# Optimization experiments

Hardware: AMD Instinct MI355X
Metric: run time of the kernel (lower is better)

Reference implementation:

```python
import jax, jax.numpy as jnp
import numpy as np

N_HEADS = 64
HEAD_DIM = 128
TOPK = 2048
CHUNK = 256          # indexer_max_chunk_size analogue (Q-block chunking)
FP8_MAX = 448.0      # e4m3 max


def _hadamard_matrix(n):
    H = np.array([[1.0]], dtype=np.float32)
    while H.shape[0] < n:
        H = np.block([[H, H], [H, -H]])
    return jnp.asarray(H, dtype=jnp.float32)

_HM = _hadamard_matrix(HEAD_DIM)


def rotate_activation(x):
    # hadamard_transform(x, scale=hidden^-0.5)
    return (x @ _HM) * (HEAD_DIM ** -0.5)


def _fp8_quant(x):
    # per-last-dim-block (block == head_dim == 128) dynamic fp8 e4m3 quantization
    amax = jnp.max(jnp.abs(x), axis=-1, keepdims=True)
    scale = jnp.maximum(amax, 1e-4) / FP8_MAX
    xq = (x / scale).astype(jnp.float8_e4m3fn).astype(jnp.float32)
    # straight-through: value == quantized, gradient == identity
    xq = x / scale + jax.lax.stop_gradient(xq - x / scale)
    return xq, scale


def setup_inputs() -> dict:
    key = jax.random.key(0)
    k1, k2, k3 = jax.random.split(key, 3)
    T = 4096
    q = jax.random.normal(k1, (T, N_HEADS, HEAD_DIM), dtype=jnp.float32)
    k = jax.random.normal(k2, (T, HEAD_DIM), dtype=jnp.float32)
    weights = jax.random.uniform(k3, (T, N_HEADS), dtype=jnp.float32)
    seq_lens = jnp.full((2,), 2048, dtype=jnp.int32)  # 2 packed sequences
    return {"q": q, "k": k, "weights": weights, "seq_lens": seq_lens}


def reference(q, k, weights, seq_lens):
    T, H, D = q.shape

    # 1) Hadamard rotation of q and k activations
    qr = rotate_activation(q)           # [T, H, D]
    kr = rotate_activation(k)           # [T, D]

    # 2) fp8 quantization with per-(token,head) / per-token scales
    qf, q_scale = _fp8_quant(qr)        # qf [T,H,D], q_scale [T,H,1]
    kf, k_scale = _fp8_quant(kr)        # kf [T,D],   k_scale [T,1]

    # 3) _scale: fold q scales + softmax scale into routing weights
    softmax_scale = D ** -0.5
    w = weights * q_scale[..., 0] * softmax_scale   # [T, H]

    # 4) causal KV bounds per packed token (compute_cu_seqlen_kv_bounds_nocache)
    offs = jnp.concatenate([jnp.zeros(1, jnp.int32), jnp.cumsum(seq_lens).astype(jnp.int32)])
    batch_ids = jnp.repeat(jnp.arange(seq_lens.shape[0], dtype=jnp.int32), seq_lens,
                           total_repeat_length=T)
    cu_ks = offs[batch_ids]                          # start of own sequence
    pos = jnp.arange(T, dtype=jnp.int32)
    cu_ke = pos + 1                                  # causal end (exclusive)

    # 5) chunked indexer logits: I[t,s] = k_scale[s] * sum_h w[t,h]*relu(qf[t,h]Âkf[s])
    n_chunks = T // CHUNK
    q_chunks = qf.reshape(n_chunks, CHUNK, H, D)
    w_chunks = w.reshape(n_chunks, CHUNK, H)

    def body(carry, inp):
        qc, wc = inp                                  # [C,H,D], [C,H]
        sc = jnp.einsum('chd,sd->chs', qc, kf)        # fp8-style GEMM
        lc = jnp.einsum('ch,chs->cs', wc, jax.nn.relu(sc))
        return carry, lc

    _, lg = jax.lax.scan(body, None, (q_chunks, w_chunks))
    logits = lg.reshape(T, T) * k_scale[:, 0][None, :]

    # 6) causal mask from bounds, then top-k KV selection
    mask = (pos[None, :] >= cu_ks[:, None]) & (pos[None, :] < cu_ke[:, None])
    masked = jnp.where(mask, logits, -jnp.inf)
    _, topk_idx = jax.lax.top_k(masked, TOPK)
    return masked, topk_idx.astype(jnp.int32)
```

## Files before the change

### kernel.cpp

```cpp
#include <hip/hip_runtime.h>
#include <stdint.h>

#define HEADS 64
#define HD 128
#define TOPK_N 2048
#define BT 32
#define BS 256
#define XCAP 256

typedef float f32x4 __attribute__((ext_vector_type(4)));
typedef long  lx2  __attribute__((ext_vector_type(2)));

static constexpr float RSQRT_D = 0.08838834764831845f;

__device__ inline unsigned short pk_fp8(float a, float b) {
    int r = __builtin_amdgcn_cvt_pk_fp8_f32(a, b, 0, false);
    return (unsigned short)(r & 0xffff);
}

__device__ inline int perm_src_lane(int m) {
    return ((m & 0x0C) << 2) | ((m & 0x30) >> 2) | (m & 3);
}

__device__ inline void fwht128(float& a, float& b, int lane) {
    float na = a + b, nb = a - b;
    a = na; b = nb;
#pragma unroll
    for (int m = 1; m < 64; m <<= 1) {
        float pa = __shfl_xor(a, m, 64);
        float pb = __shfl_xor(b, m, 64);
        bool hi = (lane & m) != 0;
        a = hi ? (pa - a) : (a + pa);
        b = hi ? (pb - b) : (b + pb);
    }
}

__global__ __launch_bounds__(256)
void k_rotquant(const float* __restrict__ kin, uint8_t* __restrict__ kf,
                float* __restrict__ k_scale, int T) {
    int wave = (int)((blockIdx.x * blockDim.x + threadIdx.x) >> 6);
    int lane = threadIdx.x & 63;
    if (wave >= T) return;
    const float2 v = ((const float2*)(kin + (size_t)wave * HD))[lane];
    float a = v.x, b = v.y;
    fwht128(a, b, lane);
    a *= RSQRT_D; b *= RSQRT_D;
    float amax = fmaxf(fabsf(a), fabsf(b));
#pragma unroll
    for (int m = 1; m < 64; m <<= 1) amax = fmaxf(amax, __shfl_xor(amax, m, 64));
    float scale = fmaxf(amax, 1e-4f) / 448.0f;
    int pk = (int)pk_fp8(a / scale, b / scale);
    int g = __shfl(pk, perm_src_lane(lane), 64);
    *(unsigned short*)(kf + (size_t)wave * HD + lane * 2) = (unsigned short)g;
    if (lane == 0) k_scale[wave] = scale;
}

__global__ __launch_bounds__(256)
void q_rotquant(const float* __restrict__ q, const float* __restrict__ weights,
                uint8_t* __restrict__ qh, float* __restrict__ wprime, int T) {
    int row = (int)((blockIdx.x * blockDim.x + threadIdx.x) >> 6);
    int lane = threadIdx.x & 63;
    if (row >= T * HEADS) return;
    int t = row >> 6, h = row & 63;
    const float2 v = ((const float2*)(q + (size_t)row * HD))[lane];
    float a = v.x, b = v.y;
    fwht128(a, b, lane);
    a *= RSQRT_D; b *= RSQRT_D;
    float amax = fmaxf(fabsf(a), fabsf(b));
#pragma unroll
    for (int m = 1; m < 64; m <<= 1) amax = fmaxf(amax, __shfl_xor(amax, m, 64));
    float scale = fmaxf(amax, 1e-4f) / 448.0f;
    int tb = t >> 5, r = t & 31;
    int pk = (int)pk_fp8(a / scale, b / scale);
    int g = __shfl(pk, perm_src_lane(lane), 64);
    size_t dst = ((((size_t)tb * HEADS + h) << 5) + r) * HD + lane * 2;
    *(unsigned short*)(qh + dst) = (unsigned short)g;
    if (lane == 0) wprime[row] = (weights[row] * scale) * RSQRT_D;
}

__global__ void bounds_kernel(const int* __restrict__ seq_lens, int B,
                              int* __restrict__ cu_ks, int T) {
    __shared__ int offs[130];
    if (threadIdx.x == 0) {
        int acc = 0; offs[0] = 0;
        for (int b = 0; b < B && b < 128; b++) { acc += seq_lens[b]; offs[b + 1] = acc; }
    }
    __syncthreads();
    int t = blockIdx.x * blockDim.x + threadIdx.x;
    if (t < T) {
        int b = 0;
        while (b < B - 1 && offs[b + 1] <= t) b++;
        cu_ks[t] = offs[b];
    }
}

__global__ __launch_bounds__(128)
void queue_kernel(const int* __restrict__ cu_ks, int* __restrict__ tiles,
                  int* __restrict__ cnt, int T) {
    int nb = T / BT;
    int tid = threadIdx.x;
    int x = tid >> 4, i = tid & 15;
    int y = i * 8 + x;
    int c = 0, sbmin = 0;
    if (y < nb) {
        int t0 = y * BT;
        sbmin = cu_ks[t0] / BS;
        c = (t0 + BT - 1) / BS - sbmin + 1;
    }
    unsigned int incl = (unsigned int)c;
#pragma unroll
    for (int o = 1; o < 16; o <<= 1) {
        unsigned int v = __shfl_up(incl, o, 16);
        if (i >= o) incl += v;
    }
    unsigned int excl = incl - (unsigned int)c;
    if (y < nb)
        for (int k = 0; k < c; k++)
            tiles[x * XCAP + excl + k] = (y << 8) | (sbmin + k);
    if (i == 15) cnt[x] = (int)incl;
}

__global__ __launch_bounds__(256)
void gemm_kernel(const uint8_t* __restrict__ qh, const uint8_t* __restrict__ kf,
                 const float* __restrict__ wprime, const float* __restrict__ k_scale,
                 const int* __restrict__ tiles, const int* __restrict__ cnt,
                 float* __restrict__ outF, int T) {
    int x = blockIdx.x & 7, j = blockIdx.x >> 3;
    if (j >= cnt[x]) return;
    int tile = tiles[x * XCAP + j];
    int y = tile >> 8, sb = tile & 255;
    int t0 = y * BT, s0 = sb * BS;

    int tid = threadIdx.x, lane = tid & 63, w = tid >> 6;
    int wr = w >> 1, wc = w & 1;
    int lrow = lane & 15, lk = lane >> 4;

    __shared__ float wlds[HEADS * BT];
    {
        const float* src = wprime + (size_t)t0 * HEADS;
        for (int i = tid; i < HEADS * BT; i += 256) {
            wlds[(i & 63) * BT + (i >> 6)] = src[i];
        }
    }
    __syncthreads();

    const f32x4 zero4 = {0.f, 0.f, 0.f, 0.f};
    const size_t HS = BT * HD;

    int rt = t0 + wr * 16;
    int cs = s0 + wc * 128;
    int tmax = t0 + BT - 1;
    int ntv = ((tmax - cs) >> 4) + 1;
    if (ntv > 8) ntv = 8;
    if (ntv <= 0) return;

    long bfrag[8][4];
#pragma unroll
    for (int nt = 0; nt < 8; nt++) {
        const uint8_t* bp = kf + (size_t)(cs + nt * 16 + lrow) * HD + lk * 32;
        lx2 b01 = *(const lx2*)(bp);
        lx2 b23 = *(const lx2*)(bp + 16);
        bfrag[nt][0] = b01.x; bfrag[nt][1] = b01.y;
        bfrag[nt][2] = b23.x; bfrag[nt][3] = b23.y;
    }

    f32x4 acc[8];
#pragma unroll
    for (int nt = 0; nt < 8; nt++) acc[nt] = zero4;

    const uint8_t* abase = qh + ((((size_t)(t0 >> 5) * HEADS) << 5)
                                 + (wr * 16 + lrow)) * HD + lk * 32;
    const float* wvbase = wlds + (size_t)(wr * 16 + lk * 4);

#define LOADA(j, hh) { const uint8_t* qp = abase + (size_t)(hh) * HS; \
        pa[j] = *(const lx2*)(qp); pb[j] = *(const lx2*)(qp + 16); }
#define COMP(j, hh) { \
        f32x4 wv = *(const f32x4*)(wvbase + ((hh) << 5)); \
        f32x4 sc[8]; \
        _Pragma("unroll") \
        for (int nt = 0; nt < 8; nt++) \
            sc[nt] = __builtin_amdgcn_mfma_f32_16x16x32_fp8_fp8(pa[j].x, bfrag[nt][0], zero4, 0, 0, 0); \
        _Pragma("unroll") \
        for (int nt = 0; nt < 8; nt++) \
            sc[nt] = __builtin_amdgcn_mfma_f32_16x16x32_fp8_fp8(pa[j].y, bfrag[nt][1], sc[nt], 0, 0, 0); \
        _Pragma("unroll") \
        for (int nt = 0; nt < 8; nt++) \
            sc[nt] = __builtin_amdgcn_mfma_f32_16x16x32_fp8_fp8(pb[j].x, bfrag[nt][2], sc[nt], 0, 0, 0); \
        _Pragma("unroll") \
        for (int nt = 0; nt < 8; nt++) \
            sc[nt] = __builtin_amdgcn_mfma_f32_16x16x32_fp8_fp8(pb[j].y, bfrag[nt][3], sc[nt], 0, 0, 0); \
        _Pragma("unroll") \
        for (int nt = 0; nt < 8; nt++) \
            acc[nt] += wv * __builtin_elementwise_max(sc[nt], zero4); \
    }

    lx2 pa[4], pb[4];
#pragma unroll
    for (int j = 0; j < 4; j++) LOADA(j, j);

    for (int h = 0; h < HEADS; h += 4) {
#pragma unroll
        for (int j = 0; j < 4; j++) {
            COMP(j, h + j);
            LOADA(j, (h + 4 + j) & 63);
        }
    }
#undef LOADA
#undef COMP

#pragma unroll
    for (int nt = 0; nt < 8; nt++) if (nt < ntv) {
        int s = cs + nt * 16 + lrow;
        float ksc = k_scale[s];
#pragma unroll
        for (int r = 0; r < 4; r++) {
            int t = rt + lk * 4 + r;
            outF[(size_t)t * T + s] = acc[nt][r] * ksc;
        }
    }
}

__global__ __launch_bounds__(256)
void sort_kernel(const float* __restrict__ outF, const int* __restrict__ cu_ks,
                 int* __restrict__ outI, int T) {
    int t = blockIdx.x;
    int tid = threadIdx.x, lane = tid & 63, wv = tid >> 6;
    int ks = cu_ks[t];
    int n = t - ks + 1;

    __shared__ unsigned long long pkB[2048];
    __shared__ unsigned int hist[2048];
    __shared__ float fred[8];
    __shared__ unsigned int wpart[4];
    __shared__ float svmax, sscale;

    const float* row = outF + (size_t)t * T + ks;

    float vmin = 3.4e38f, vmax = -3.4e38f;
    for (int i = tid; i < n; i += 256) {
        float v = row[i];
        vmin = fminf(vmin, v); vmax = fmaxf(vmax, v);
    }
#pragma unroll
    for (int o = 1; o < 64; o <<= 1) {
        vmin = fminf(vmin, __shfl_xor(vmin, o, 64));
        vmax = fmaxf(vmax, __shfl_xor(vmax, o, 64));
    }
    if (lane == 0) { fred[wv] = vmin; fred[4 + wv] = vmax; }
    for (int i = tid; i < 2048; i += 256) hist[i] = 0;
    __syncthreads();
    if (tid == 0) {
        float mn = fred[0], mx = fred[4];
#pragma unroll
        for (int j = 1; j < 4; j++) { mn = fminf(mn, fred[j]); mx = fmaxf(mx, fred[4 + j]); }
        float range = mx - mn;
        svmax = mx;
        sscale = (range > 0.f) ? (2047.0f / range) : 0.f;
    }
    __syncthreads();
    const float vmx = svmax, scl = sscale;

    for (int i = tid; i < n; i += 256) {
        unsigned int b = (unsigned int)((vmx - row[i]) * scl);
        if (b > 2047u) b = 2047u;
        atomicAdd(&hist[b], 1u);
    }
    __syncthreads();

    unsigned int hloc[8], s8 = 0;
#pragma unroll
    for (int k = 0; k < 8; k++) { hloc[k] = hist[tid * 8 + k]; s8 += hloc[k]; }
    unsigned int incl = s8;
#pragma unroll
    for (int o = 1; o < 64; o <<= 1) {
        unsigned int v = __shfl_up(incl, o, 64);
        if (lane >= o) incl += v;
    }
    if (lane == 63) wpart[wv] = incl;
    __syncthreads();
    unsigned int base = 0;
#pragma unroll
    for (int j = 0; j < 4; j++) base += (j < wv) ? wpart[j] : 0;
    unsigned int run = base + incl - s8;
#pragma unroll
    for (int k = 0; k < 8; k++) { hist[tid * 8 + k] = run; run += hloc[k]; }
    __syncthreads();

    for (int i = tid; i < n; i += 256) {
        float v = row[i];
        unsigned int u = __float_as_uint(v);
        unsigned int asc = u ^ ((u >> 31) ? 0xFFFFFFFFu : 0x80000000u);
        unsigned int dk = ~asc;
        unsigned int b = (unsigned int)((vmx - v) * scl);
        if (b > 2047u) b = 2047u;
        unsigned int pos = atomicAdd(&hist[b], 1u);
        pkB[pos] = ((unsigned long long)dk << 32) | (unsigned int)i;
    }
    __syncthreads();

    for (int b = tid; b < 2048; b += 256) {
        int e = (int)hist[b];
        int s = (b == 0) ? 0 : (int)hist[b - 1];
        for (int i = s + 1; i < e; i++) {
            unsigned long long key = pkB[i];
            int j = i - 1;
            while (j >= s && pkB[j] > key) { pkB[j + 1] = pkB[j]; j--; }
            pkB[j + 1] = key;
        }
    }
    __syncthreads();

    for (int j = tid; j < TOPK_N; j += 256) {
        int v;
        if (j < n) v = ks + (int)(pkB[j] & 0xFFFFu);
        else { int f = j - n; v = (f < ks) ? f : (t + 1) + (f - ks); }
        outI[(size_t)t * TOPK_N + j] = v;
    }
}

extern "C" void kernel_launch(void* const* d_in, const int* in_sizes, int n_in,
                              void* d_out, int out_size, void* d_ws, size_t ws_size,
                              hipStream_t stream) {
    const float* q       = (const float*)d_in[0];
    const float* k       = (const float*)d_in[1];
    const float* weights = (const float*)d_in[2];
    const int* seq_lens  = (const int*)d_in[3];

    int T = in_sizes[1] / HD;
    int B = in_sizes[3];

    uint8_t* ws = (uint8_t*)d_ws;
    size_t off = 0;
    uint8_t* kf    = ws;                    off += (size_t)T * HD;
    float* k_scale = (float*)(ws + off);    off += (size_t)T * 4;
    float* wprime  = (float*)(ws + off);    off += (size_t)T * HEADS * 4;
    uint8_t* qh    = ws + off;              off += (size_t)T * HEADS * HD;
    int* cu_ks     = (int*)(ws + off);      off += (size_t)T * 4;
    int* tiles     = (int*)(ws + off);      off += (size_t)8 * XCAP * 4;
    int* cnt       = (int*)(ws + off);      off += 64;

    float* outF = (float*)d_out;
    int* outI   = (int*)d_out + (size_t)T * T;

    k_rotquant<<<(T + 3) / 4, 256, 0, stream>>>(k, kf, k_scale, T);
    q_rotquant<<<(T * HEADS + 3) / 4, 256, 0, stream>>>(q, weights, qh, wprime, T);
    bounds_kernel<<<(T + 255) / 256, 256, 0, stream>>>(seq_lens, B, cu_ks, T);
    queue_kernel<<<1, 128, 0, stream>>>(cu_ks, tiles, cnt, T);

    gemm_kernel<<<2048, 256, 0, stream>>>(qh, kf, wprime, k_scale, tiles, cnt, outF, T);

    sort_kernel<<<T, 256, 0, stream>>>(outF, cu_ks, outI, T);
}
```

Measured before the change: 190.2 us.

## Fuse row min/max into GEMM epilogue and vectorize q rotation-quant

The GEMM epilogue now computes per-row min and max of the logits it writes. It reduces them across lanes and publishes them with atomicMin/atomicMax on order-preserving encoded floats. This lets the sort kernel skip its separate pass over each row to find the histogram range. q_rotquant is also restructured to handle four rows per wave with eight elements per lane, doing part of the Hadamard in registers and writing 64-bit fp8 stores, which cuts shuffles. The trade-off is extra atomics and init work. Tiles may also include out-of-mask columns in the min/max, which widens the histogram range and makes the bins coarser.

```diff
diff --git a/kernel.cpp b/kernel.cpp
--- a/kernel.cpp
+++ b/kernel.cpp
@@ -16,6 +16,15 @@
 __device__ inline unsigned short pk_fp8(float a, float b) {
     int r = __builtin_amdgcn_cvt_pk_fp8_f32(a, b, 0, false);
     return (unsigned short)(r & 0xffff);
+}
+
+__device__ inline unsigned enc_f(float f) {
+    unsigned u = __float_as_uint(f);
+    return u ^ ((unsigned)((int)u >> 31) | 0x80000000u);
+}
+__device__ inline float dec_f(unsigned e) {
+    return (e & 0x80000000u) ? __uint_as_float(e ^ 0x80000000u)
+                             : __uint_as_float(~e);
 }
 
 __device__ inline int perm_src_lane(int m) {
@@ -58,28 +67,61 @@
 __global__ __launch_bounds__(256)
 void q_rotquant(const float* __restrict__ q, const float* __restrict__ weights,
                 uint8_t* __restrict__ qh, float* __restrict__ wprime, int T) {
-    int row = (int)((blockIdx.x * blockDim.x + threadIdx.x) >> 6);
+    int gwave = (int)((blockIdx.x * blockDim.x + threadIdx.x) >> 6);
     int lane = threadIdx.x & 63;
+    int l16 = lane & 15, sub = lane >> 4;
+    int row = gwave * 4 + sub;
     if (row >= T * HEADS) return;
     int t = row >> 6, h = row & 63;
-    const float2 v = ((const float2*)(q + (size_t)row * HD))[lane];
-    float a = v.x, b = v.y;
-    fwht128(a, b, lane);
-    a *= RSQRT_D; b *= RSQRT_D;
-    float amax = fmaxf(fabsf(a), fabsf(b));
-#pragma unroll
-    for (int m = 1; m < 64; m <<= 1) amax = fmaxf(amax, __shfl_xor(amax, m, 64));
+
+    const float4* src = (const float4*)(q + (size_t)row * HD + l16 * 8);
+    float4 x0 = src[0], x1 = src[1];
+    float v[8] = {x0.x, x0.y, x0.z, x0.w, x1.x, x1.y, x1.z, x1.w};
+
+#pragma unroll
+    for (int s = 1; s <= 4; s <<= 1) {
+        float nv[8];
+#pragma unroll
+        for (int e = 0; e < 8; e++)
+            nv[e] = (e & s) ? (v[e ^ s] - v[e]) : (v[e] + v[e ^ s]);
+#pragma unroll
+        for (int e = 0; e < 8; e++) v[e] = nv[e];
+    }
+#pragma unroll
+    for (int m = 1; m <= 8; m <<= 1) {
+        bool hi = (l16 & m) != 0;
+#pragma unroll
+        for (int e = 0; e < 8; e++) {
+            float pv = __shfl_xor(v[e], m, 64);
+            v[e] = hi ? (pv - v[e]) : (v[e] + pv);
+        }
+    }
+    float amax = 0.f;
+#pragma unroll
+    for (int e = 0; e < 8; e++) {
+        v[e] *= RSQRT_D;
+        amax = fmaxf(amax, fabsf(v[e]));
+    }
+#pragma unroll
+    for (int m = 1; m <= 8; m <<= 1)
+        amax = fmaxf(amax, __shfl_xor(amax, m, 64));
     float scale = fmaxf(amax, 1e-4f) / 448.0f;
+
+    unsigned long long w64 =
+          (unsigned long long)pk_fp8(v[0] / scale, v[1] / scale)
+        | ((unsigned long long)pk_fp8(v[2] / scale, v[3] / scale) << 16)
+        | ((unsigned long long)pk_fp8(v[4] / scale, v[5] / scale) << 32)
+        | ((unsigned long long)pk_fp8(v[6] / scale, v[7] / scale) << 48);
+
     int tb = t >> 5, r = t & 31;
-    int pk = (int)pk_fp8(a / scale, b / scale);
-    int g = __shfl(pk, perm_src_lane(lane), 64);
-    size_t dst = ((((size_t)tb * HEADS + h) << 5) + r) * HD + lane * 2;
-    *(unsigned short*)(qh + dst) = (unsigned short)g;
-    if (lane == 0) wprime[row] = (weights[row] * scale) * RSQRT_D;
+    size_t base = ((((size_t)tb * HEADS + h) << 5) + r) * HD;
+    *(unsigned long long*)(qh + base + (l16 & 3) * 32 + ((l16 >> 2) << 3)) = w64;
+    if (l16 == 0) wprime[row] = (weights[row] * scale) * RSQRT_D;
 }
 
 __global__ void bounds_kernel(const int* __restrict__ seq_lens, int B,
-                              int* __restrict__ cu_ks, int T) {
+                              int* __restrict__ cu_ks, unsigned* __restrict__ rkmin,
+                              unsigned* __restrict__ rkmax, int T) {
     __shared__ int offs[130];
     if (threadIdx.x == 0) {
         int acc = 0; offs[0] = 0;
@@ -91,6 +133,8 @@
         int b = 0;
         while (b < B - 1 && offs[b + 1] <= t) b++;
         cu_ks[t] = offs[b];
+        rkmin[t] = 0xFFFFFFFFu;
+        rkmax[t] = 0u;
     }
 }
 
@@ -124,6 +168,7 @@
 void gemm_kernel(const uint8_t* __restrict__ qh, const uint8_t* __restrict__ kf,
                  const float* __restrict__ wprime, const float* __restrict__ k_scale,
                  const int* __restrict__ tiles, const int* __restrict__ cnt,
+                 unsigned* __restrict__ rkmin, unsigned* __restrict__ rkmax,
                  float* __restrict__ outF, int T) {
     int x = blockIdx.x & 7, j = blockIdx.x >> 3;
     if (j >= cnt[x]) return;
@@ -208,20 +253,41 @@
 #undef LOADA
 #undef COMP
 
+    float mnv[4] = {3.4e38f, 3.4e38f, 3.4e38f, 3.4e38f};
+    float mxv[4] = {-3.4e38f, -3.4e38f, -3.4e38f, -3.4e38f};
 #pragma unroll
     for (int nt = 0; nt < 8; nt++) if (nt < ntv) {
         int s = cs + nt * 16 + lrow;
         float ksc = k_scale[s];
 #pragma unroll
         for (int r = 0; r < 4; r++) {
+            float val = acc[nt][r] * ksc;
+            outF[(size_t)(rt + lk * 4 + r) * T + s] = val;
+            mnv[r] = fminf(mnv[r], val);
+            mxv[r] = fmaxf(mxv[r], val);
+        }
+    }
+#pragma unroll
+    for (int r = 0; r < 4; r++) {
+#pragma unroll
+        for (int o = 1; o < 16; o <<= 1) {
+            mnv[r] = fminf(mnv[r], __shfl_xor(mnv[r], o, 64));
+            mxv[r] = fmaxf(mxv[r], __shfl_xor(mxv[r], o, 64));
+        }
+    }
+    if (lrow == 0) {
+#pragma unroll
+        for (int r = 0; r < 4; r++) {
             int t = rt + lk * 4 + r;
-            outF[(size_t)t * T + s] = acc[nt][r] * ksc;
+            atomicMin(&rkmin[t], enc_f(mnv[r]));
+            atomicMax(&rkmax[t], enc_f(mxv[r]));
         }
     }
 }
 
 __global__ __launch_bounds__(256)
 void sort_kernel(const float* __restrict__ outF, const int* __restrict__ cu_ks,
+                 const unsigned* __restrict__ rkmin, const unsigned* __restrict__ rkmax,
                  int* __restrict__ outI, int T) {
     int t = blockIdx.x;
     int tid = threadIdx.x, lane = tid & 63, wv = tid >> 6;
@@ -230,29 +296,15 @@
 
     __shared__ unsigned long long pkB[2048];
     __shared__ unsigned int hist[2048];
-    __shared__ float fred[8];
     __shared__ unsigned int wpart[4];
     __shared__ float svmax, sscale;
 
     const float* row = outF + (size_t)t * T + ks;
 
-    float vmin = 3.4e38f, vmax = -3.4e38f;
-    for (int i = tid; i < n; i += 256) {
-        float v = row[i];
-        vmin = fminf(vmin, v); vmax = fmaxf(vmax, v);
-    }
-#pragma unroll
-    for (int o = 1; o < 64; o <<= 1) {
-        vmin = fminf(vmin, __shfl_xor(vmin, o, 64));
-        vmax = fmaxf(vmax, __shfl_xor(vmax, o, 64));
-    }
-    if (lane == 0) { fred[wv] = vmin; fred[4 + wv] = vmax; }
     for (int i = tid; i < 2048; i += 256) hist[i] = 0;
-    __syncthreads();
     if (tid == 0) {
-        float mn = fred[0], mx = fred[4];
-#pragma unroll
-        for (int j = 1; j < 4; j++) { mn = fminf(mn, fred[j]); mx = fmaxf(mx, fred[4 + j]); }
+        float mx = dec_f(rkmax[t]);
+        float mn = dec_f(rkmin[t]);
         float range = mx - mn;
         svmax = mx;
         sscale = (range > 0.f) ? (2047.0f / range) : 0.f;
@@ -338,16 +390,19 @@
     int* cu_ks     = (int*)(ws + off);      off += (size_t)T * 4;
     int* tiles     = (int*)(ws + off);      off += (size_t)8 * XCAP * 4;
     int* cnt       = (int*)(ws + off);      off += 64;
+    unsigned* rkmin = (unsigned*)(ws + off); off += (size_t)T * 4;
+    unsigned* rkmax = (unsigned*)(ws + off); off += (size_t)T * 4;
 
     float* outF = (float*)d_out;
     int* outI   = (int*)d_out + (size_t)T * T;
 
     k_rotquant<<<(T + 3) / 4, 256, 0, stream>>>(k, kf, k_scale, T);
-    q_rotquant<<<(T * HEADS + 3) / 4, 256, 0, stream>>>(q, weights, qh, wprime, T);
-    bounds_kernel<<<(T + 255) / 256, 256, 0, stream>>>(seq_lens, B, cu_ks, T);
+    q_rotquant<<<(T * HEADS + 15) / 16, 256, 0, stream>>>(q, weights, qh, wprime, T);
+    bounds_kernel<<<(T + 255) / 256, 256, 0, stream>>>(seq_lens, B, cu_ks, rkmin, rkmax, T);
     queue_kernel<<<1, 128, 0, stream>>>(cu_ks, tiles, cnt, T);
 
-    gemm_kernel<<<2048, 256, 0, stream>>>(qh, kf, wprime, k_scale, tiles, cnt, outF, T);
-
-    sort_kernel<<<T, 256, 0, stream>>>(outF, cu_ks, outI, T);
-}
+    gemm_kernel<<<2048, 256, 0, stream>>>(qh, kf, wprime, k_scale, tiles, cnt,
+                                          rkmin, rkmax, outF, T);
+
+    sort_kernel<<<T, 256, 0, stream>>>(outF, cu_ks, rkmin, rkmax, outI, T);
+}
```

Result: faster. 162.2 us (-14.7%).
